# Performance work log

Measured on AMD Instinct MI355X. Metric: run time of the kernel, lower is better.

The kernel has to match this reference:

```python
import jax, jax.numpy as jnp
import numpy as np

GROUP_SIZES = np.array([64, 48, 56, 40, 32, 24, 16, 8])
N_GROUPS = 8
MAX_GS = 64
D_MODEL = 2048
BATCH = 8192


def setup_inputs() -> dict:
    key = jax.random.key(0)
    k1, k2, k3, k4 = jax.random.split(key, 4)
    hidden = jax.random.normal(k1, (BATCH, N_GROUPS, D_MODEL), dtype=jnp.float32)
    chosen = jax.random.randint(k2, (BATCH,), 0, N_GROUPS)
    scale = 1.0 / np.sqrt(D_MODEL)  # nn.Linear default init range
    W = jax.random.uniform(k3, (N_GROUPS, MAX_GS, D_MODEL), minval=-scale, maxval=scale, dtype=jnp.float32)
    b = jax.random.uniform(k4, (N_GROUPS, MAX_GS), minval=-scale, maxval=scale, dtype=jnp.float32)
    gs = jnp.asarray(GROUP_SIZES, dtype=jnp.int32)
    # zero-pad decoder rows beyond each group's true output size
    row_mask = jnp.arange(MAX_GS)[None, :] < gs[:, None]  # [G, MAX_GS]
    W = W * row_mask[:, :, None]
    b = b * row_mask
    return {"hidden": hidden, "chosen_group_idx": chosen, "W": W, "b": b, "group_sizes": gs}


def reference(hidden, chosen_group_idx, W, b, group_sizes):
    # hidden: [B, G, D]; chosen_group_idx: [B]; W: [G, MAX_GS, D] (zero-padded); b: [G, MAX_GS]
    # Gather each sample's chosen group slice: [B, D]
    h = jnp.take_along_axis(hidden, chosen_group_idx[:, None, None], axis=1)[:, 0, :]
    Wg = W[chosen_group_idx]  # [B, MAX_GS, D]
    bg = b[chosen_group_idx]  # [B, MAX_GS]
    preds = jnp.einsum('bd,bgd->bg', h, Wg) + bg  # [B, MAX_GS]
    valid = jnp.arange(W.shape[1])[None, :] < group_sizes[chosen_group_idx][:, None]
    preds = jnp.where(valid, preds, 0.0)  # padded slots are zero, as in the torch module
    return preds, valid
```

## Files before the change

### kernel.cpp

```cpp
#include <hip/hip_runtime.h>
#include <hip/hip_bf16.h>

#define BATCH   8192
#define NGRP    8
#define MAXGS   64
#define DMODEL  2048
#define TM      16
#define NBLK    32
#define NKK     (DMODEL / 32)
#define MAXTILES 520

typedef __attribute__((ext_vector_type(8))) short  short8;
typedef __attribute__((ext_vector_type(4))) float  f32x4;
typedef __attribute__((ext_vector_type(4))) short  short4v;

#define CNT_OFF   0
#define HIST_OFF  512
#define MAP_OFF   1536
#define LISTS_OFF 4096
#define W_OFF     (LISTS_OFF + NGRP * BATCH * 4)
#define CNT_STRIDE 16

static __device__ __forceinline__ short bf(float f) {
    __hip_bfloat16 h = __float2bfloat16(f);
    return (short)__bfloat16_as_ushort(h);
}

__global__ __launch_bounds__(256) void init_hist_kernel(
    const float* __restrict__ W,
    const int* __restrict__ chosen,
    unsigned short* __restrict__ Wb2,
    int* __restrict__ hist)
{
    int blk = blockIdx.x;
    int tid = threadIdx.x;
    if (blk < 1024) {
        int e = (blk * 256 + tid) * 4;
        int g = e >> 17;
        int rem = e & ((MAXGS * DMODEL) - 1);
        int c = rem >> 11;
        int k = rem & (DMODEL - 1);
        int kk = k >> 5, j = k & 31;
        float4 w = *reinterpret_cast<const float4*>(W + e);
        ushort4 o;
        o.x = (unsigned short)bf(w.x); o.y = (unsigned short)bf(w.y);
        o.z = (unsigned short)bf(w.z); o.w = (unsigned short)bf(w.w);
        size_t dst = (((size_t)g * NKK + kk) * MAXGS + c) * 32 + j;
        *reinterpret_cast<ushort4*>(Wb2 + dst) = o;
    } else {
        int hb = blk - 1024;
        __shared__ int h[NGRP];
        if (tid < NGRP) h[tid] = 0;
        __syncthreads();
        int g = chosen[hb * 256 + tid];
        atomicAdd(&h[g], 1);
        __syncthreads();
        if (tid < NGRP) hist[hb * NGRP + tid] = h[tid];
    }
}

__global__ __launch_bounds__(256) void scatter_kernel(const int* __restrict__ chosen,
                                                      const int* __restrict__ hist,
                                                      int* __restrict__ lists,
                                                      int* __restrict__ cnt,
                                                      int* __restrict__ map) {
    __shared__ int hloc[NBLK * NGRP];
    __shared__ int gbase[NGRP];
    __shared__ int ntl[NGRP];
    __shared__ int wcnt[4][NGRP];
    __shared__ int wbase[4][NGRP];
    int tid  = threadIdx.x;
    int blk  = blockIdx.x;
    int w    = tid >> 6;
    int lane = tid & 63;

    if (tid < NBLK * NGRP) hloc[tid] = hist[tid];
    __syncthreads();
    if (tid < NGRP) {
        int s = 0;
        for (int b2 = 0; b2 < blk; ++b2) s += hloc[b2 * NGRP + tid];
        gbase[tid] = s;
        int tot = s;
        for (int b2 = blk; b2 < NBLK; ++b2) tot += hloc[b2 * NGRP + tid];
        ntl[tid] = (tot + TM - 1) / TM;
        if (blk == 0) cnt[tid * CNT_STRIDE] = tot;
    }
    __syncthreads();

    if (blk == 0) {
        for (int q = tid; q < MAXTILES; q += 256) map[q] = -1;
        __syncthreads();
        for (int p = tid; p < NGRP * 512; p += 256) {
            int t = p >> 3, gg = p & 7;
            if (t < ntl[gg]) {
                int pos = 0;
                #pragma unroll
                for (int g2 = 0; g2 < NGRP; ++g2) {
                    int nt = ntl[g2];
                    pos += (t < nt ? t : nt);
                    pos += (g2 < gg && nt > t) ? 1 : 0;
                }
                map[pos] = (gg << 16) | t;
            }
        }
    }

    int b = blk * 256 + tid;
    int g = chosen[b];
    int rank = 0;
    unsigned long long below = (1ull << lane) - 1ull;
    #pragma unroll
    for (int gg = 0; gg < NGRP; ++gg) {
        unsigned long long m = __ballot(g == gg);
        if (g == gg) rank = __popcll(m & below);
        if (lane == gg) wcnt[w][gg] = __popcll(m);
    }
    __syncthreads();
    if (tid < NGRP) {
        int base = gbase[tid];
        #pragma unroll
        for (int ww = 0; ww < 4; ++ww) {
            wbase[ww][tid] = base;
            base += wcnt[ww][tid];
        }
    }
    __syncthreads();
    lists[g * BATCH + wbase[w][g] + rank] = b;
}

__global__ __launch_bounds__(256, 2) void gemm_kernel(
    const float* __restrict__ hidden,
    const float* __restrict__ bias,
    const int* __restrict__ gsizes,
    const int* __restrict__ cnt,
    const int* __restrict__ lists,
    const int* __restrict__ map,
    const unsigned short* __restrict__ Wb2,
    float* __restrict__ out)
{
    int e = map[blockIdx.x];
    if (e < 0) return;
    int g = e >> 16;
    int t = e & 0xFFFF;
    int c = cnt[g * CNT_STRIDE];
    int m0 = t * TM;

    __shared__ unsigned short A[TM][DMODEL];

    int tid  = threadIdx.x;
    int w    = tid >> 6;
    int lane = tid & 63;
    int lrow = lane & 15;
    int kg   = lane >> 4;

    {
        const float* src[4];
        #pragma unroll
        for (int i = 0; i < 4; ++i) {
            int m  = m0 + 4 * w + i;
            int ms = m < c ? m : c - 1;
            src[i] = hidden + ((size_t)lists[g * BATCH + ms] * NGRP + g) * DMODEL
                   + lane * 4;
        }
        f32x4 ra[8], rb[8];
        #pragma unroll
        for (int h = 0; h < 8; ++h)
            ra[h] = *reinterpret_cast<const f32x4*>(src[0] + h * 256);
        #pragma unroll
        for (int h = 0; h < 8; ++h)
            rb[h] = *reinterpret_cast<const f32x4*>(src[1] + h * 256);

        #pragma unroll
        for (int i = 0; i < 4; ++i) {
            int r = 4 * w + i;
            int swz = ((r & 7) << 4) | ((r & 1) << 6);
            char* abase = (char*)&A[r][0];
            #pragma unroll
            for (int h = 0; h < 8; ++h) {
                f32x4 v = ra[h];
                short4v o;
                o[0] = bf(v[0]); o[1] = bf(v[1]); o[2] = bf(v[2]); o[3] = bf(v[3]);
                int byte = (h * 512 + lane * 8) ^ swz;
                *reinterpret_cast<short4v*>(abase + byte) = o;
            }
            if (i < 3) {
                #pragma unroll
                for (int h = 0; h < 8; ++h) ra[h] = rb[h];
                if (i < 2) {
                    #pragma unroll
                    for (int h = 0; h < 8; ++h)
                        rb[h] = *reinterpret_cast<const f32x4*>(src[i + 2] + h * 256);
                }
            }
        }
    }
    __syncthreads();

    {
        int swzr = ((lrow & 7) << 4) | ((lrow & 1) << 6);
        const char* arow = (const char*)&A[lrow][0];
        const unsigned short* bp =
            Wb2 + (size_t)g * NKK * MAXGS * 32 + (w * 16 + lrow) * 32 + kg * 8;

        f32x4 acc = f32x4{0, 0, 0, 0};
        #pragma unroll 8
        for (int kk = 0; kk < NKK; ++kk) {
            int byte = (kk * 64 + kg * 16) ^ swzr;
            short8 af  = *reinterpret_cast<const short8*>(arow + byte);
            short8 bfr = *reinterpret_cast<const short8*>(bp + (size_t)kk * MAXGS * 32);
            acc = __builtin_amdgcn_mfma_f32_16x16x32_bf16(af, bfr, acc, 0, 0, 0);
        }

        int gsz = gsizes[g];
        int n = w * 16 + lrow;
        float bv = bias[g * MAXGS + n];
        #pragma unroll
        for (int r = 0; r < 4; ++r) {
            int m = m0 + kg * 4 + r;
            if (m < c) {
                int s = lists[g * BATCH + m];
                out[(size_t)s * MAXGS + n] = acc[r] + bv;
                out[(size_t)(BATCH + s) * MAXGS + n] = (n < gsz) ? 1.0f : 0.0f;
            }
        }
    }
}

extern "C" void kernel_launch(void* const* d_in, const int* in_sizes, int n_in,
                              void* d_out, int out_size, void* d_ws, size_t ws_size,
                              hipStream_t stream) {
    const float* hidden = (const float*)d_in[0];
    const int*   chosen = (const int*)d_in[1];
    const float* W      = (const float*)d_in[2];
    const float* bias   = (const float*)d_in[3];
    const int*   gs     = (const int*)d_in[4];
    float* out = (float*)d_out;

    char* ws = (char*)d_ws;
    int* cnt   = (int*)(ws + CNT_OFF);
    int* hist  = (int*)(ws + HIST_OFF);
    int* map   = (int*)(ws + MAP_OFF);
    int* lists = (int*)(ws + LISTS_OFF);
    unsigned short* Wb2 = (unsigned short*)(ws + W_OFF);

    init_hist_kernel<<<dim3(1024 + NBLK), dim3(256), 0, stream>>>(W, chosen, Wb2, hist);
    scatter_kernel<<<dim3(NBLK), dim3(256), 0, stream>>>(chosen, hist, lists, cnt, map);
    gemm_kernel<<<dim3(MAXTILES), dim3(256), 0, stream>>>(
        hidden, bias, gs, cnt, lists, map, Wb2, out);
}
```

Measured before the change: 38.29 us.

## Double-buffer A staging over K chunks to overlap loads with MFMA

Splits the K dimension of the gathered hidden rows into four chunks of 512 and stages them through a double-buffered shared-memory tile, so the global loads and bf16 conversion for the next chunk overlap with MFMAs on the current one. Shared memory per block drops from 64KB to 32KB and launch bounds rise to 4 blocks per CU for higher occupancy. The swizzle pattern is changed to suit the smaller row width. The cost is a barrier per chunk and a register budget that must fit the higher occupancy target.

After: 37.36 us. 2.4% less time.

```diff
diff --git a/kernel.cpp b/kernel.cpp
--- a/kernel.cpp
+++ b/kernel.cpp
@@ -8,11 +8,13 @@
 #define TM      16
 #define NBLK    32
 #define NKK     (DMODEL / 32)
+#define KC      512
+#define NCH     (DMODEL / KC)
+#define KKP     (KC / 32)
 #define MAXTILES 520
 
 typedef __attribute__((ext_vector_type(8))) short  short8;
 typedef __attribute__((ext_vector_type(4))) float  f32x4;
-typedef __attribute__((ext_vector_type(4))) short  short4v;
 
 #define CNT_OFF   0
 #define HIST_OFF  512
@@ -128,7 +130,7 @@
     lists[g * BATCH + wbase[w][g] + rank] = b;
 }
 
-__global__ __launch_bounds__(256, 2) void gemm_kernel(
+__global__ __launch_bounds__(256, 4) void gemm_kernel(
     const float* __restrict__ hidden,
     const float* __restrict__ bias,
     const int* __restrict__ gsizes,
@@ -145,7 +147,7 @@
     int c = cnt[g * CNT_STRIDE];
     int m0 = t * TM;
 
-    __shared__ unsigned short A[TM][DMODEL];
+    __shared__ unsigned short A[2][TM][KC];
 
     int tid  = threadIdx.x;
     int w    = tid >> 6;
@@ -153,75 +155,68 @@
     int lrow = lane & 15;
     int kg   = lane >> 4;
 
-    {
-        const float* src[4];
+    const float* src[4];
+    #pragma unroll
+    for (int i = 0; i < 4; ++i) {
+        int m  = m0 + 4 * w + i;
+        int ms = m < c ? m : c - 1;
+        src[i] = hidden + ((size_t)lists[g * BATCH + ms] * NGRP + g) * DMODEL
+               + lane * 8;
+    }
+
+    auto STAGE = [&](int buf, int ch) {
+        f32x4 v0[4], v1[4];
         #pragma unroll
         for (int i = 0; i < 4; ++i) {
-            int m  = m0 + 4 * w + i;
-            int ms = m < c ? m : c - 1;
-            src[i] = hidden + ((size_t)lists[g * BATCH + ms] * NGRP + g) * DMODEL
-                   + lane * 4;
-        }
-        f32x4 ra[8], rb[8];
-        #pragma unroll
-        for (int h = 0; h < 8; ++h)
-            ra[h] = *reinterpret_cast<const f32x4*>(src[0] + h * 256);
-        #pragma unroll
-        for (int h = 0; h < 8; ++h)
-            rb[h] = *reinterpret_cast<const f32x4*>(src[1] + h * 256);
-
+            v0[i] = *reinterpret_cast<const f32x4*>(src[i] + ch * KC);
+            v1[i] = *reinterpret_cast<const f32x4*>(src[i] + ch * KC + 4);
+        }
         #pragma unroll
         for (int i = 0; i < 4; ++i) {
             int r = 4 * w + i;
-            int swz = ((r & 7) << 4) | ((r & 1) << 6);
-            char* abase = (char*)&A[r][0];
-            #pragma unroll
-            for (int h = 0; h < 8; ++h) {
-                f32x4 v = ra[h];
-                short4v o;
-                o[0] = bf(v[0]); o[1] = bf(v[1]); o[2] = bf(v[2]); o[3] = bf(v[3]);
-                int byte = (h * 512 + lane * 8) ^ swz;
-                *reinterpret_cast<short4v*>(abase + byte) = o;
-            }
-            if (i < 3) {
-                #pragma unroll
-                for (int h = 0; h < 8; ++h) ra[h] = rb[h];
-                if (i < 2) {
-                    #pragma unroll
-                    for (int h = 0; h < 8; ++h)
-                        rb[h] = *reinterpret_cast<const f32x4*>(src[i + 2] + h * 256);
-                }
-            }
-        }
-    }
-    __syncthreads();
-
-    {
-        int swzr = ((lrow & 7) << 4) | ((lrow & 1) << 6);
-        const char* arow = (const char*)&A[lrow][0];
-        const unsigned short* bp =
-            Wb2 + (size_t)g * NKK * MAXGS * 32 + (w * 16 + lrow) * 32 + kg * 8;
-
-        f32x4 acc = f32x4{0, 0, 0, 0};
+            int swz = ((r & 3) << 4) | (((r >> 3) & 1) << 6);
+            short8 o;
+            o[0] = bf(v0[i][0]); o[1] = bf(v0[i][1]);
+            o[2] = bf(v0[i][2]); o[3] = bf(v0[i][3]);
+            o[4] = bf(v1[i][0]); o[5] = bf(v1[i][1]);
+            o[6] = bf(v1[i][2]); o[7] = bf(v1[i][3]);
+            char* ab = (char*)&A[buf][r][0];
+            *reinterpret_cast<short8*>(ab + ((lane * 16) ^ swz)) = o;
+        }
+    };
+
+    int swzr = ((lrow & 3) << 4) | (((lrow >> 3) & 1) << 6);
+    const unsigned short* bp =
+        Wb2 + (size_t)g * NKK * MAXGS * 32 + (w * 16 + lrow) * 32 + kg * 8;
+    f32x4 acc = f32x4{0, 0, 0, 0};
+
+    STAGE(0, 0);
+    __syncthreads();
+    #pragma unroll
+    for (int ch = 0; ch < NCH; ++ch) {
+        if (ch + 1 < NCH) STAGE((ch + 1) & 1, ch + 1);
+        const char* abase = (const char*)&A[ch & 1][lrow][0];
         #pragma unroll 8
-        for (int kk = 0; kk < NKK; ++kk) {
-            int byte = (kk * 64 + kg * 16) ^ swzr;
-            short8 af  = *reinterpret_cast<const short8*>(arow + byte);
-            short8 bfr = *reinterpret_cast<const short8*>(bp + (size_t)kk * MAXGS * 32);
+        for (int k2 = 0; k2 < KKP; ++k2) {
+            int byte = (k2 * 64 + kg * 16) ^ swzr;
+            short8 af  = *reinterpret_cast<const short8*>(abase + byte);
+            short8 bfr = *reinterpret_cast<const short8*>(
+                bp + (size_t)(ch * KKP + k2) * MAXGS * 32);
             acc = __builtin_amdgcn_mfma_f32_16x16x32_bf16(af, bfr, acc, 0, 0, 0);
         }
-
-        int gsz = gsizes[g];
-        int n = w * 16 + lrow;
-        float bv = bias[g * MAXGS + n];
-        #pragma unroll
-        for (int r = 0; r < 4; ++r) {
-            int m = m0 + kg * 4 + r;
-            if (m < c) {
-                int s = lists[g * BATCH + m];
-                out[(size_t)s * MAXGS + n] = acc[r] + bv;
-                out[(size_t)(BATCH + s) * MAXGS + n] = (n < gsz) ? 1.0f : 0.0f;
-            }
+        __syncthreads();
+    }
+
+    int gsz = gsizes[g];
+    int n = w * 16 + lrow;
+    float bv = bias[g * MAXGS + n];
+    #pragma unroll
+    for (int r = 0; r < 4; ++r) {
+        int m = m0 + kg * 4 + r;
+        if (m < c) {
+            int s = lists[g * BATCH + m];
+            out[(size_t)s * MAXGS + n] = acc[r] + bv;
+            out[(size_t)(BATCH + s) * MAXGS + n] = (n < gsz) ? 1.0f : 0.0f;
         }
     }
 }
```
